# Optimization experiments

Hardware: AMD Instinct MI355X
Metric: run time of the kernel (lower is better)

Reference implementation:

```python
import jax, jax.numpy as jnp
import numpy as np

DIM = 2048
HEAD_DIM = 128
N_HEADS = 16
N_KV = 4
THETA = 10000.0
M = 2
B = 2
S = 2048


def _rope_table(seq_len, head_dim, theta):
    half = head_dim // 2
    inv_freq = 1.0 / (theta ** (jnp.arange(half, dtype=jnp.float32) * 2.0 / head_dim))
    ang = jnp.outer(jnp.arange(seq_len, dtype=jnp.float32), inv_freq)  # [S, half]
    cos, sin = jnp.cos(ang), jnp.sin(ang)
    # [S, half, 2, 2] rotation matrices: [[cos, -sin], [sin, cos]]
    return jnp.stack([jnp.stack([cos, -sin], axis=-1), jnp.stack([sin, cos], axis=-1)], axis=-2)


def setup_inputs() -> dict:
    key = jax.random.key(0)
    ks = jax.random.split(key, 6)
    std = DIM ** -0.5
    x = jax.random.normal(ks[0], (B, S, DIM), jnp.float32)
    Wq = jax.random.normal(ks[1], (M, DIM, N_HEADS * HEAD_DIM), jnp.float32) * std
    Wk = jax.random.normal(ks[2], (M, M, DIM, N_KV * HEAD_DIM), jnp.float32) * std
    Wv = jax.random.normal(ks[3], (M, M, DIM, N_KV * HEAD_DIM), jnp.float32) * std
    Wo = jax.random.normal(ks[4], (M, N_HEADS * HEAD_DIM, DIM), jnp.float32) * std
    modality_ids = jax.random.randint(ks[5], (B, S), 0, M, dtype=jnp.int32)
    freq_cis = _rope_table(S, HEAD_DIM, THETA)
    return {"x": x, "freq_cis": freq_cis, "Wq": Wq, "Wk": Wk, "Wv": Wv, "Wo": Wo,
            "modality_ids": modality_ids}


def _select_by_modality(all_proj, mid):
    # all_proj: [B, S, M, E]; mid: [B, S] int -> [B, S, E]
    Bb, Ss, Mm, E = all_proj.shape
    idx = jnp.broadcast_to(mid[:, :, None, None].astype(jnp.int32), (Bb, Ss, 1, E))
    return jnp.take_along_axis(all_proj, idx, axis=2)[:, :, 0]


def reference(x, freq_cis, Wq, Wk, Wv, Wo, modality_ids):
    Bb, Ss, D = x.shape
    mid = modality_ids

    # Per-modality Q projection, then per-token selection (gather/scatter in torch).
    q_all = jnp.einsum('bsd,mde->bsme', x, Wq)  # [B,S,M,H*hd]
    xq = _select_by_modality(q_all, mid)

    # In the original, xk[src token] accumulates wk[src_to_tgt](x) over ALL tgt,
    # which by linearity equals x @ sum_tgt(Wk[src, tgt]).
    Wk_sum = Wk.sum(axis=1)  # [M, D, Kh*hd]
    Wv_sum = Wv.sum(axis=1)
    k_all = jnp.einsum('bsd,mde->bsme', x, Wk_sum)
    v_all = jnp.einsum('bsd,mde->bsme', x, Wv_sum)
    xk = _select_by_modality(k_all, mid)
    xv = _select_by_modality(v_all, mid)

    xq = xq.reshape(Bb, Ss, N_HEADS, HEAD_DIM)
    xk = xk.reshape(Bb, Ss, N_KV, HEAD_DIM)
    xv = xv.reshape(Bb, Ss, N_KV, HEAD_DIM)

    # RoPE (positions = arange since tok_idx is None)
    F = freq_cis[:Ss]  # [S, hd/2, 2, 2]

    def rope(t):
        th = t.reshape(t.shape[0], t.shape[1], t.shape[2], HEAD_DIM // 2, 2)
        return jnp.einsum('bshdp,sdpq->bshdq', th, F).reshape(t.shape)

    xq = rope(xq)
    xk = rope(xk)

    # GQA repeat (interleaved, matching expand+reshape)
    rep = N_HEADS // N_KV
    xk = jnp.repeat(xk, rep, axis=2)
    xv = jnp.repeat(xv, rep, axis=2)

    q = xq.transpose(0, 2, 1, 3)  # [B,H,S,hd]
    k = xk.transpose(0, 2, 1, 3)
    v = xv.transpose(0, 2, 1, 3)

    scale = 1.0 / jnp.sqrt(jnp.asarray(HEAD_DIM, dtype=q.dtype))
    scores = jnp.einsum('bhqd,bhkd->bhqk', q, k) * scale
    attn = jax.nn.softmax(scores, axis=-1)
    out = jnp.einsum('bhqk,bhkd->bqhd', attn, v).reshape(Bb, Ss, N_HEADS * HEAD_DIM)

    # Per-modality output projection + selection
    o_all = jnp.einsum('bse,med->bsmd', out, Wo)  # [B,S,M,D]
    final = _select_by_modality(o_all, mid)
    return final
```

## Files before the change

### kernel.cpp

```cpp
#include <hip/hip_runtime.h>
#include <hip/hip_bf16.h>
#include <stdint.h>

typedef unsigned short u16;
typedef __attribute__((ext_vector_type(8))) __bf16 bf16x8;
typedef __attribute__((ext_vector_type(4))) float f32x4;
typedef __attribute__((ext_vector_type(8))) u16 us8;

#define QSCALE 0.08838834764831843f

__device__ __forceinline__ u16 f2bf(float f) {
  unsigned u = __float_as_uint(f);
  u += 0x7fffu + ((u >> 16) & 1u);
  return (u16)(u >> 16);
}
__device__ __forceinline__ float bf2f(u16 h) {
  return __uint_as_float(((unsigned)h) << 16);
}
__device__ __forceinline__ void gload16(const void* g, void* l) {
  __builtin_amdgcn_global_load_lds(
      (const __attribute__((address_space(1))) unsigned int*)g,
      (__attribute__((address_space(3))) unsigned int*)l, 16, 0, 0);
}

__global__ __launch_bounds__(256) void wprep(
    const float* __restrict__ Wq, const float* __restrict__ Wk,
    const float* __restrict__ Wv, const float* __restrict__ Wo,
    u16* __restrict__ WCT, u16* __restrict__ WOT) {
  const int sec = blockIdx.z;
  const float* s0;
  const float* s1 = nullptr;
  u16* dst;
  int N;
  switch (sec) {
    case 0: s0 = Wq;                 dst = WCT;               N = 2048; break;
    case 1: s0 = Wq + 2048*2048;     dst = WCT + 2048*2048;   N = 2048; break;
    case 2: s0 = Wk;                 s1 = Wk + 2048*512;      dst = WCT + 4096*2048; N = 512; break;
    case 3: s0 = Wk + 2*2048*512;    s1 = Wk + 3*2048*512;    dst = WCT + 4608*2048; N = 512; break;
    case 4: s0 = Wv;                 s1 = Wv + 2048*512;      dst = WCT + 5120*2048; N = 512; break;
    case 5: s0 = Wv + 2*2048*512;    s1 = Wv + 3*2048*512;    dst = WCT + 5632*2048; N = 512; break;
    case 6: s0 = Wo;                 dst = WOT;               N = 2048; break;
    default: s0 = Wo + 2048*2048;    dst = WOT + 2048*2048;   N = 2048; break;
  }
  const int n0 = blockIdx.x * 32;
  if (n0 >= N) return;
  const int k0 = blockIdx.y * 32;
  __shared__ float tile[32][33];
  const int tx = threadIdx.x & 31, ty = threadIdx.x >> 5;
#pragma unroll
  for (int i = 0; i < 4; ++i) {
    int k = k0 + ty + 8 * i;
    float v = s0[(size_t)k * N + n0 + tx];
    if (s1) v += s1[(size_t)k * N + n0 + tx];
    tile[ty + 8 * i][tx] = v;
  }
  __syncthreads();
#pragma unroll
  for (int i = 0; i < 4; ++i) {
    int n = n0 + ty + 8 * i;
    dst[(size_t)n * 2048 + k0 + tx] = f2bf(tile[tx][ty + 8 * i]);
  }
}

__global__ __launch_bounds__(256) void xcast(const float* __restrict__ x,
                                             u16* __restrict__ Xbf) {
  size_t base = ((size_t)blockIdx.x * 256 + threadIdx.x) * 8;
  float4 a = *(const float4*)&x[base];
  float4 c = *(const float4*)&x[base + 4];
  us8 o;
  o[0] = f2bf(a.x); o[1] = f2bf(a.y); o[2] = f2bf(a.z); o[3] = f2bf(a.w);
  o[4] = f2bf(c.x); o[5] = f2bf(c.y); o[6] = f2bf(c.z); o[7] = f2bf(c.w);
  *(us8*)&Xbf[base] = o;
}

__global__ __launch_bounds__(256) void gemm_bt(
    const u16* __restrict__ A, const u16* __restrict__ B, u16* __restrict__ C,
    int Mdim, int Ndim, int Kdim) {
  __shared__ u16 As[128 * 32];
  __shared__ u16 Bs[128 * 32];
  const int nbx = gridDim.x;
  const int nwg = nbx * gridDim.y;
  int bid = blockIdx.y * nbx + blockIdx.x;
  const int q = nwg >> 3;
  int swz = (bid & 7) * q + (bid >> 3);
  const int bx = swz % nbx, by = swz / nbx;
  const int row0 = by * 128, col0 = bx * 128;
  const int tid = threadIdx.x, wid = tid >> 6, lane = tid & 63;
  const int lr = lane & 15, lg = lane >> 4;
  const int wr = wid >> 1, wc = wid & 1;
  const u16* Abase = A + (size_t)row0 * Kdim;
  const u16* Bbase = B + (size_t)col0 * Kdim;

  f32x4 acc[4][4];
#pragma unroll
  for (int m = 0; m < 4; ++m)
#pragma unroll
    for (int n = 0; n < 4; ++n)
#pragma unroll
      for (int r = 0; r < 4; ++r) acc[m][n][r] = 0.f;

  for (int k0 = 0; k0 < Kdim; k0 += 32) {
#pragma unroll
    for (int j = 0; j < 2; ++j) {
      int c = j * 256 + wid * 64 + lane;
      int r = c >> 2, g = c & 3;
      gload16(Abase + (size_t)r * Kdim + k0 + g * 8, &As[(j * 256 + wid * 64) * 8]);
      gload16(Bbase + (size_t)r * Kdim + k0 + g * 8, &Bs[(j * 256 + wid * 64) * 8]);
    }
    __syncthreads();
    bf16x8 af[4], bfr[4];
#pragma unroll
    for (int m = 0; m < 4; ++m)
      af[m] = *(const bf16x8*)&As[(64 * wr + 16 * m + lr) * 32 + 8 * lg];
#pragma unroll
    for (int n = 0; n < 4; ++n)
      bfr[n] = *(const bf16x8*)&Bs[(64 * wc + 16 * n + lr) * 32 + 8 * lg];
#pragma unroll
    for (int m = 0; m < 4; ++m)
#pragma unroll
      for (int n = 0; n < 4; ++n)
        acc[m][n] = __builtin_amdgcn_mfma_f32_16x16x32_bf16(af[m], bfr[n], acc[m][n], 0, 0, 0);
    __syncthreads();
  }
#pragma unroll
  for (int m = 0; m < 4; ++m)
#pragma unroll
    for (int n = 0; n < 4; ++n)
#pragma unroll
      for (int r = 0; r < 4; ++r) {
        int grow = row0 + 64 * wr + 16 * m + 4 * lg + r;
        int gcol = col0 + 64 * wc + 16 * n + lr;
        C[(size_t)grow * Ndim + gcol] = f2bf(acc[m][n][r]);
      }
}

__global__ __launch_bounds__(256) void gemm_out(
    const u16* __restrict__ A, const u16* __restrict__ B,
    const int* __restrict__ mid, float* __restrict__ out) {
  __shared__ u16 As[128 * 32];
  __shared__ u16 Bs[128 * 32];
  const int nbx = gridDim.x;
  const int nwg = nbx * gridDim.y;
  int bid = blockIdx.y * nbx + blockIdx.x;
  const int q = nwg >> 3;
  int swz = (bid & 7) * q + (bid >> 3);
  const int bx = swz % nbx, by = swz / nbx;
  const int row0 = by * 128, col0 = bx * 128;
  const int tid = threadIdx.x, wid = tid >> 6, lane = tid & 63;
  const int lr = lane & 15, lg = lane >> 4;
  const int wr = wid >> 1, wc = wid & 1;
  const u16* Abase = A + (size_t)row0 * 2048;
  const u16* Bbase = B + (size_t)col0 * 2048;

  f32x4 acc[4][4];
#pragma unroll
  for (int m = 0; m < 4; ++m)
#pragma unroll
    for (int n = 0; n < 4; ++n)
#pragma unroll
      for (int r = 0; r < 4; ++r) acc[m][n][r] = 0.f;

  for (int k0 = 0; k0 < 2048; k0 += 32) {
#pragma unroll
    for (int j = 0; j < 2; ++j) {
      int c = j * 256 + wid * 64 + lane;
      int r = c >> 2, g = c & 3;
      gload16(Abase + (size_t)r * 2048 + k0 + g * 8, &As[(j * 256 + wid * 64) * 8]);
      gload16(Bbase + (size_t)r * 2048 + k0 + g * 8, &Bs[(j * 256 + wid * 64) * 8]);
    }
    __syncthreads();
    bf16x8 af[4], bfr[4];
#pragma unroll
    for (int m = 0; m < 4; ++m)
      af[m] = *(const bf16x8*)&As[(64 * wr + 16 * m + lr) * 32 + 8 * lg];
#pragma unroll
    for (int n = 0; n < 4; ++n)
      bfr[n] = *(const bf16x8*)&Bs[(64 * wc + 16 * n + lr) * 32 + 8 * lg];
#pragma unroll
    for (int m = 0; m < 4; ++m)
#pragma unroll
      for (int n = 0; n < 4; ++n)
        acc[m][n] = __builtin_amdgcn_mfma_f32_16x16x32_bf16(af[m], bfr[n], acc[m][n], 0, 0, 0);
    __syncthreads();
  }
#pragma unroll
  for (int m = 0; m < 4; ++m)
#pragma unroll
    for (int n = 0; n < 4; ++n)
#pragma unroll
      for (int r = 0; r < 4; ++r) {
        int grow = row0 + 64 * wr + 16 * m + 4 * lg + r;
        int gcol = col0 + 64 * wc + 16 * n + lr;
        int mod = gcol >> 11;
        if (mid[grow] == mod)
          out[(size_t)grow * 2048 + (gcol & 2047)] = acc[m][n][r];
      }
}

__global__ __launch_bounds__(256) void rope_select(
    const u16* __restrict__ QKV, const int* __restrict__ mid,
    const float* __restrict__ fc, u16* __restrict__ Qr, u16* __restrict__ Kr) {
  const int t = blockIdx.x;
  const int b = t >> 11, s = t & 2047;
  const int m = mid[t];
  __shared__ float Fs[256];
  Fs[threadIdx.x] = fc[(size_t)s * 256 + threadIdx.x];
  __syncthreads();
  const int tid = threadIdx.x;
  {
    int p0 = tid * 4;
    int h = p0 >> 6, ph0 = p0 & 63;
    const u16* src = QKV + (size_t)t * 6144 + m * 2048 + h * 128 + 2 * ph0;
    us8 v = *(const us8*)src;
    us8 o;
#pragma unroll
    for (int j = 0; j < 4; ++j) {
      float x0 = bf2f(v[2 * j]), x1 = bf2f(v[2 * j + 1]);
      const float* F = &Fs[(ph0 + j) * 4];
      o[2 * j]     = f2bf((x0 * F[0] + x1 * F[2]) * QSCALE);
      o[2 * j + 1] = f2bf((x0 * F[1] + x1 * F[3]) * QSCALE);
    }
    *(us8*)(Qr + (((size_t)(b * 16 + h) * 2048) + s) * 128 + 2 * ph0) = o;
  }
  if (tid < 64) {
    int p0 = tid * 4;
    int kh = p0 >> 6, ph0 = p0 & 63;
    const u16* src = QKV + (size_t)t * 6144 + 4096 + m * 512 + kh * 128 + 2 * ph0;
    us8 v = *(const us8*)src;
    us8 o;
#pragma unroll
    for (int j = 0; j < 4; ++j) {
      float x0 = bf2f(v[2 * j]), x1 = bf2f(v[2 * j + 1]);
      const float* F = &Fs[(ph0 + j) * 4];
      o[2 * j]     = f2bf(x0 * F[0] + x1 * F[2]);
      o[2 * j + 1] = f2bf(x0 * F[1] + x1 * F[3]);
    }
    *(us8*)(Kr + (((size_t)(b * 4 + kh) * 2048) + s) * 128 + 2 * ph0) = o;
  }
}

__global__ __launch_bounds__(256) void vtrans(
    const u16* __restrict__ QKV, const int* __restrict__ mid, u16* __restrict__ Vt) {
  __shared__ u16 tilebuf[32][34];
  const int s0 = blockIdx.x * 32, d0 = blockIdx.y * 32, b = blockIdx.z;
  const int tx = threadIdx.x & 31, ty = threadIdx.x >> 5;
#pragma unroll
  for (int i = 0; i < 4; ++i) {
    int s = s0 + ty + 8 * i;
    int t = b * 2048 + s;
    int m = mid[t];
    tilebuf[ty + 8 * i][tx] = QKV[(size_t)t * 6144 + 5120 + m * 512 + d0 + tx];
  }
  __syncthreads();
#pragma unroll
  for (int i = 0; i < 4; ++i) {
    int d = d0 + ty + 8 * i;
    Vt[(((size_t)(b * 4 + (d >> 7)) * 128) + (d & 127)) * 2048 + s0 + tx] =
        tilebuf[tx][ty + 8 * i];
  }
}

__global__ __launch_bounds__(256) void attn(
    const u16* __restrict__ Qr, const u16* __restrict__ Kr,
    const u16* __restrict__ Vt, u16* __restrict__ AO) {
  __shared__ u16 Ks[64 * 128];
  __shared__ u16 Vs[128 * 64];
  __shared__ u16 Ps[4][16 * 64];
  const int qb = blockIdx.x, h = blockIdx.y, b = blockIdx.z;
  const int kvh = h >> 2;
  const int tid = threadIdx.x, wid = tid >> 6, lane = tid & 63;
  const int lr = lane & 15, lg = lane >> 4;
  const u16* qp = Qr + (((size_t)(b * 16 + h) * 2048) + qb * 64 + 16 * wid) * 128;
  const u16* kp = Kr + ((size_t)(b * 4 + kvh) * 2048) * 128;
  const u16* vp = Vt + ((size_t)(b * 4 + kvh) * 128) * 2048;

  bf16x8 qf[4];
#pragma unroll
  for (int t4 = 0; t4 < 4; ++t4)
    qf[t4] = *(const bf16x8*)(qp + (size_t)lr * 128 + 32 * t4 + 8 * lg);

  f32x4 o[8];
#pragma unroll
  for (int i = 0; i < 8; ++i)
#pragma unroll
    for (int r = 0; r < 4; ++r) o[i][r] = 0.f;
  float mrow[4] = {-1e30f, -1e30f, -1e30f, -1e30f};
  float lrow[4] = {0.f, 0.f, 0.f, 0.f};

  for (int kb = 0; kb < 2048; kb += 64) {
#pragma unroll
    for (int j = 0; j < 4; ++j) {
      int c = j * 256 + wid * 64 + lane;
      int rk = c >> 4, gk = (c & 15) ^ (rk & 7);
      gload16(kp + (size_t)(kb + rk) * 128 + gk * 8, &Ks[(j * 256 + wid * 64) * 8]);
      int rv = c >> 3, gv = (c & 7) ^ (rv & 7);
      gload16(vp + (size_t)rv * 2048 + kb + gv * 8, &Vs[(j * 256 + wid * 64) * 8]);
    }
    __syncthreads();

    f32x4 s[4];
#pragma unroll
    for (int nf = 0; nf < 4; ++nf)
#pragma unroll
      for (int r = 0; r < 4; ++r) s[nf][r] = 0.f;
#pragma unroll
    for (int nf = 0; nf < 4; ++nf) {
      int R = 16 * nf + lr;
#pragma unroll
      for (int t4 = 0; t4 < 4; ++t4) {
        bf16x8 kf = *(const bf16x8*)&Ks[R * 128 + (((4 * t4 + lg) ^ (R & 7)) * 8)];
        s[nf] = __builtin_amdgcn_mfma_f32_16x16x32_bf16(qf[t4], kf, s[nf], 0, 0, 0);
      }
    }
    float sc[4];
#pragma unroll
    for (int r = 0; r < 4; ++r) {
      float mx = fmaxf(fmaxf(s[0][r], s[1][r]), fmaxf(s[2][r], s[3][r]));
      mx = fmaxf(mx, __shfl_xor(mx, 1));
      mx = fmaxf(mx, __shfl_xor(mx, 2));
      mx = fmaxf(mx, __shfl_xor(mx, 4));
      mx = fmaxf(mx, __shfl_xor(mx, 8));
      float mn = fmaxf(mrow[r], mx);
      sc[r] = __expf(mrow[r] - mn);
      float ps = 0.f;
#pragma unroll
      for (int nf = 0; nf < 4; ++nf) {
        float e = __expf(s[nf][r] - mn);
        s[nf][r] = e;
        ps += e;
      }
      ps += __shfl_xor(ps, 1);
      ps += __shfl_xor(ps, 2);
      ps += __shfl_xor(ps, 4);
      ps += __shfl_xor(ps, 8);
      lrow[r] = lrow[r] * sc[r] + ps;
      mrow[r] = mn;
    }
#pragma unroll
    for (int i = 0; i < 8; ++i)
#pragma unroll
      for (int r = 0; r < 4; ++r) o[i][r] *= sc[r];
    u16* pw = Ps[wid];
#pragma unroll
    for (int nf = 0; nf < 4; ++nf) {
      int cg = 2 * nf + (lr >> 3), ci = lr & 7;
#pragma unroll
      for (int r = 0; r < 4; ++r) {
        int prow = 4 * lg + r;
        pw[prow * 64 + ((cg ^ (prow & 7)) * 8) + ci] = f2bf(s[nf][r]);
      }
    }
#pragma unroll
    for (int ks = 0; ks < 2; ++ks) {
      bf16x8 pa = *(const bf16x8*)&pw[lr * 64 + (((4 * ks + lg) ^ (lr & 7)) * 8)];
#pragma unroll
      for (int n2 = 0; n2 < 8; ++n2) {
        int R2 = 16 * n2 + lr;
        bf16x8 vf = *(const bf16x8*)&Vs[R2 * 64 + (((4 * ks + lg) ^ (R2 & 7)) * 8)];
        o[n2] = __builtin_amdgcn_mfma_f32_16x16x32_bf16(pa, vf, o[n2], 0, 0, 0);
      }
    }
    __syncthreads();
  }
#pragma unroll
  for (int n2 = 0; n2 < 8; ++n2)
#pragma unroll
    for (int r = 0; r < 4; ++r) {
      int qrow = qb * 64 + 16 * wid + 4 * lg + r;
      AO[((size_t)(b * 2048) + qrow) * 2048 + h * 128 + 16 * n2 + lr] =
          f2bf(o[n2][r] / lrow[r]);
    }
}

extern "C" void kernel_launch(void* const* d_in, const int* in_sizes, int n_in,
                              void* d_out, int out_size, void* d_ws, size_t ws_size,
                              hipStream_t stream) {
  const float* x  = (const float*)d_in[0];
  const float* fc = (const float*)d_in[1];
  const float* Wq = (const float*)d_in[2];
  const float* Wk = (const float*)d_in[3];
  const float* Wv = (const float*)d_in[4];
  const float* Wo = (const float*)d_in[5];
  const int* mid  = (const int*)d_in[6];
  float* out = (float*)d_out;
  char* ws = (char*)d_ws;

  u16* XBF = (u16*)(ws);
  u16* WCT = (u16*)(ws + 16777216);
  u16* WOT = (u16*)(ws + 41943040);
  u16* QKV = (u16*)(ws + 58720256);
  u16* QR  = (u16*)(ws + 109051904);
  u16* KR  = (u16*)(ws + 125829120);
  u16* VT  = (u16*)(ws + 130023424);
  u16* AO  = (u16*)(ws + 134217728);
  if (ws_size < 150994944) return;

  wprep<<<dim3(64, 64, 8), dim3(256), 0, stream>>>(Wq, Wk, Wv, Wo, WCT, WOT);
  xcast<<<dim3(4096), dim3(256), 0, stream>>>(x, XBF);
  gemm_bt<<<dim3(48, 32), dim3(256), 0, stream>>>(XBF, WCT, QKV, 4096, 6144, 2048);
  rope_select<<<dim3(4096), dim3(256), 0, stream>>>(QKV, mid, fc, QR, KR);
  vtrans<<<dim3(64, 16, 2), dim3(256), 0, stream>>>(QKV, mid, VT);
  attn<<<dim3(32, 16, 2), dim3(256), 0, stream>>>(QR, KR, VT, AO);
  gemm_out<<<dim3(32, 32), dim3(256), 0, stream>>>(AO, WOT, mid, out);
}
```

Measured before the change: 613.3 us.

## Restructure attention with 32x32 MFMA, double-buffered KV, and register-resident P

Rewrites the attention kernel so each 512-thread block handles 256 queries (32 per wave), using 32x32x16 MFMAs with S computed transposed. P is kept in registers and exchanged via a lane-32 shuffle instead of going through LDS. K/V tiles are double-buffered so the next tile's loads overlap compute, and the running-max rescale is skipped when the new max stays within a threshold. Output is staged through LDS for coalesced stores. The cost is higher register and LDS pressure, and fewer blocks in the grid.

```diff
diff --git a/kernel.cpp b/kernel.cpp
--- a/kernel.cpp
+++ b/kernel.cpp
@@ -5,7 +5,9 @@
 typedef unsigned short u16;
 typedef __attribute__((ext_vector_type(8))) __bf16 bf16x8;
 typedef __attribute__((ext_vector_type(4))) float f32x4;
+typedef __attribute__((ext_vector_type(16))) float f32x16;
 typedef __attribute__((ext_vector_type(8))) u16 us8;
+typedef __attribute__((ext_vector_type(4))) unsigned u32x4;
 
 #define QSCALE 0.08838834764831843f
 
@@ -21,6 +23,9 @@
   __builtin_amdgcn_global_load_lds(
       (const __attribute__((address_space(1))) unsigned int*)g,
       (__attribute__((address_space(3))) unsigned int*)l, 16, 0, 0);
+}
+__device__ __forceinline__ unsigned sx32(unsigned v) {
+  return (unsigned)__shfl_xor((int)v, 32, 64);
 }
 
 __global__ __launch_bounds__(256) void wprep(
@@ -260,116 +265,149 @@
   }
 }
 
-__global__ __launch_bounds__(256) void attn(
+__global__ __launch_bounds__(512, 2) void attn(
     const u16* __restrict__ Qr, const u16* __restrict__ Kr,
     const u16* __restrict__ Vt, u16* __restrict__ AO) {
-  __shared__ u16 Ks[64 * 128];
-  __shared__ u16 Vs[128 * 64];
-  __shared__ u16 Ps[4][16 * 64];
-  const int qb = blockIdx.x, h = blockIdx.y, b = blockIdx.z;
-  const int kvh = h >> 2;
-  const int tid = threadIdx.x, wid = tid >> 6, lane = tid & 63;
-  const int lr = lane & 15, lg = lane >> 4;
-  const u16* qp = Qr + (((size_t)(b * 16 + h) * 2048) + qb * 64 + 16 * wid) * 128;
+  __shared__ u16 smem[34816];
+  u16* Kbuf[2] = { smem,          smem + 16384 };
+  u16* Vbuf[2] = { smem +  8192,  smem + 24576 };
+  Kbuf[0] = smem;          Vbuf[0] = smem + 8192;
+  Kbuf[1] = smem + 16384;  Vbuf[1] = smem + 24576;
+
+  const int qt = blockIdx.x, hd = blockIdx.y, b = blockIdx.z;
+  const int kvh = hd >> 2;
+  const int tid = threadIdx.x, wid = tid >> 6;
+  const int l31 = tid & 31, h = (tid >> 5) & 1;
+  const bool hi = h != 0;
+
+  const u16* qp = Qr + (((size_t)(b * 16 + hd) * 2048) + qt * 256 + wid * 32 + l31) * 128;
   const u16* kp = Kr + ((size_t)(b * 4 + kvh) * 2048) * 128;
   const u16* vp = Vt + ((size_t)(b * 4 + kvh) * 128) * 2048;
 
-  bf16x8 qf[4];
-#pragma unroll
-  for (int t4 = 0; t4 < 4; ++t4)
-    qf[t4] = *(const bf16x8*)(qp + (size_t)lr * 128 + 32 * t4 + 8 * lg);
-
-  f32x4 o[8];
-#pragma unroll
-  for (int i = 0; i < 8; ++i)
-#pragma unroll
-    for (int r = 0; r < 4; ++r) o[i][r] = 0.f;
-  float mrow[4] = {-1e30f, -1e30f, -1e30f, -1e30f};
-  float lrow[4] = {0.f, 0.f, 0.f, 0.f};
-
+  bf16x8 qf[8];
+#pragma unroll
+  for (int ds = 0; ds < 8; ++ds)
+    qf[ds] = *(const bf16x8*)(qp + 16 * ds + 8 * h);
+
+  f32x16 oacc[4];
+#pragma unroll
+  for (int dt = 0; dt < 4; ++dt)
+#pragma unroll
+    for (int r = 0; r < 16; ++r) oacc[dt][r] = 0.f;
+  float mrun = -1e30f, lrun = 0.f;
+
+#define STAGE_KV(KB, DK, DV)                                                   \
+  {                                                                            \
+    _Pragma("unroll") for (int j = 0; j < 2; ++j) {                            \
+      int c = j * 512 + tid;                                                   \
+      int rk = c >> 4, gk = (c & 15) ^ (rk & 7);                               \
+      gload16(kp + (size_t)((KB) + rk) * 128 + gk * 8,                         \
+              (DK) + (j * 512 + wid * 64) * 8);                                \
+      int rv = c >> 3, gv = (c & 7) ^ (rv & 7);                                \
+      gload16(vp + (size_t)rv * 2048 + (KB) + gv * 8,                          \
+              (DV) + (j * 512 + wid * 64) * 8);                                \
+    }                                                                          \
+  }
+
+  STAGE_KV(0, Kbuf[0], Vbuf[0]);
+  __syncthreads();
+
+  int cur = 0;
   for (int kb = 0; kb < 2048; kb += 64) {
-#pragma unroll
-    for (int j = 0; j < 4; ++j) {
-      int c = j * 256 + wid * 64 + lane;
-      int rk = c >> 4, gk = (c & 15) ^ (rk & 7);
-      gload16(kp + (size_t)(kb + rk) * 128 + gk * 8, &Ks[(j * 256 + wid * 64) * 8]);
-      int rv = c >> 3, gv = (c & 7) ^ (rv & 7);
-      gload16(vp + (size_t)rv * 2048 + kb + gv * 8, &Vs[(j * 256 + wid * 64) * 8]);
+    const u16* Kb = Kbuf[cur];
+    const u16* Vb = Vbuf[cur];
+    if (kb + 64 < 2048) STAGE_KV(kb + 64, Kbuf[cur ^ 1], Vbuf[cur ^ 1]);
+
+    f32x16 s0, s1;
+#pragma unroll
+    for (int r = 0; r < 16; ++r) { s0[r] = 0.f; s1[r] = 0.f; }
+    const int key0 = l31, key1 = 32 + l31;
+#pragma unroll
+    for (int ds = 0; ds < 8; ++ds) {
+      bf16x8 kf0 = *(const bf16x8*)&Kb[key0 * 128 + (((2 * ds + h) ^ (key0 & 7)) * 8)];
+      s0 = __builtin_amdgcn_mfma_f32_32x32x16_bf16(kf0, qf[ds], s0, 0, 0, 0);
+      bf16x8 kf1 = *(const bf16x8*)&Kb[key1 * 128 + (((2 * ds + h) ^ (key1 & 7)) * 8)];
+      s1 = __builtin_amdgcn_mfma_f32_32x32x16_bf16(kf1, qf[ds], s1, 0, 0, 0);
+    }
+
+    float pm = -1e30f;
+#pragma unroll
+    for (int r = 0; r < 16; ++r) pm = fmaxf(pm, fmaxf(s0[r], s1[r]));
+    pm = fmaxf(pm, __shfl_xor(pm, 32, 64));
+    if (!__all(pm <= mrun + 8.f)) {
+      float mn = fmaxf(mrun, pm);
+      float sc = __expf(mrun - mn);
+      mrun = mn;
+      lrun *= sc;
+#pragma unroll
+      for (int dt = 0; dt < 4; ++dt)
+#pragma unroll
+        for (int r = 0; r < 16; ++r) oacc[dt][r] *= sc;
+    }
+    float ls = 0.f;
+#pragma unroll
+    for (int r = 0; r < 16; ++r) { s0[r] = __expf(s0[r] - mrun); ls += s0[r]; }
+#pragma unroll
+    for (int r = 0; r < 16; ++r) { s1[r] = __expf(s1[r] - mrun); ls += s1[r]; }
+    ls += __shfl_xor(ls, 32, 64);
+    lrun += ls;
+
+    unsigned c[16];
+#pragma unroll
+    for (int j = 0; j < 8; ++j) {
+      asm("v_cvt_pk_bf16_f32 %0, %1, %2" : "=v"(c[j]) : "v"(s0[2 * j]), "v"(s0[2 * j + 1]));
+      asm("v_cvt_pk_bf16_f32 %0, %1, %2" : "=v"(c[8 + j]) : "v"(s1[2 * j]), "v"(s1[2 * j + 1]));
+    }
+
+#pragma unroll
+    for (int st = 0; st < 4; ++st) {
+      unsigned w0 = sx32(c[4 * st + 0]);
+      unsigned w1 = sx32(c[4 * st + 1]);
+      unsigned w2 = sx32(c[4 * st + 2]);
+      unsigned w3 = sx32(c[4 * st + 3]);
+      u32x4 pw;
+      pw.x = hi ? w2 : c[4 * st + 0];
+      pw.y = hi ? w3 : c[4 * st + 1];
+      pw.z = hi ? c[4 * st + 2] : w0;
+      pw.w = hi ? c[4 * st + 3] : w1;
+      union { u32x4 u; bf16x8 bf; } pc;
+      pc.u = pw;
+#pragma unroll
+      for (int dt = 0; dt < 4; ++dt) {
+        int d = 32 * dt + l31;
+        bf16x8 vf = *(const bf16x8*)&Vb[d * 64 + (((2 * st + h) ^ (d & 7)) * 8)];
+        oacc[dt] = __builtin_amdgcn_mfma_f32_32x32x16_bf16(vf, pc.bf, oacc[dt], 0, 0, 0);
+      }
     }
     __syncthreads();
-
-    f32x4 s[4];
-#pragma unroll
-    for (int nf = 0; nf < 4; ++nf)
-#pragma unroll
-      for (int r = 0; r < 4; ++r) s[nf][r] = 0.f;
-#pragma unroll
-    for (int nf = 0; nf < 4; ++nf) {
-      int R = 16 * nf + lr;
-#pragma unroll
-      for (int t4 = 0; t4 < 4; ++t4) {
-        bf16x8 kf = *(const bf16x8*)&Ks[R * 128 + (((4 * t4 + lg) ^ (R & 7)) * 8)];
-        s[nf] = __builtin_amdgcn_mfma_f32_16x16x32_bf16(qf[t4], kf, s[nf], 0, 0, 0);
-      }
-    }
-    float sc[4];
-#pragma unroll
-    for (int r = 0; r < 4; ++r) {
-      float mx = fmaxf(fmaxf(s[0][r], s[1][r]), fmaxf(s[2][r], s[3][r]));
-      mx = fmaxf(mx, __shfl_xor(mx, 1));
-      mx = fmaxf(mx, __shfl_xor(mx, 2));
-      mx = fmaxf(mx, __shfl_xor(mx, 4));
-      mx = fmaxf(mx, __shfl_xor(mx, 8));
-      float mn = fmaxf(mrow[r], mx);
-      sc[r] = __expf(mrow[r] - mn);
-      float ps = 0.f;
-#pragma unroll
-      for (int nf = 0; nf < 4; ++nf) {
-        float e = __expf(s[nf][r] - mn);
-        s[nf][r] = e;
-        ps += e;
-      }
-      ps += __shfl_xor(ps, 1);
-      ps += __shfl_xor(ps, 2);
-      ps += __shfl_xor(ps, 4);
-      ps += __shfl_xor(ps, 8);
-      lrow[r] = lrow[r] * sc[r] + ps;
-      mrow[r] = mn;
-    }
-#pragma unroll
-    for (int i = 0; i < 8; ++i)
-#pragma unroll
-      for (int r = 0; r < 4; ++r) o[i][r] *= sc[r];
-    u16* pw = Ps[wid];
-#pragma unroll
-    for (int nf = 0; nf < 4; ++nf) {
-      int cg = 2 * nf + (lr >> 3), ci = lr & 7;
-#pragma unroll
-      for (int r = 0; r < 4; ++r) {
-        int prow = 4 * lg + r;
-        pw[prow * 64 + ((cg ^ (prow & 7)) * 8) + ci] = f2bf(s[nf][r]);
-      }
-    }
-#pragma unroll
-    for (int ks = 0; ks < 2; ++ks) {
-      bf16x8 pa = *(const bf16x8*)&pw[lr * 64 + (((4 * ks + lg) ^ (lr & 7)) * 8)];
-#pragma unroll
-      for (int n2 = 0; n2 < 8; ++n2) {
-        int R2 = 16 * n2 + lr;
-        bf16x8 vf = *(const bf16x8*)&Vs[R2 * 64 + (((4 * ks + lg) ^ (R2 & 7)) * 8)];
-        o[n2] = __builtin_amdgcn_mfma_f32_16x16x32_bf16(pa, vf, o[n2], 0, 0, 0);
-      }
-    }
-    __syncthreads();
-  }
-#pragma unroll
-  for (int n2 = 0; n2 < 8; ++n2)
-#pragma unroll
-    for (int r = 0; r < 4; ++r) {
-      int qrow = qb * 64 + 16 * wid + 4 * lg + r;
-      AO[((size_t)(b * 2048) + qrow) * 2048 + h * 128 + 16 * n2 + lr] =
-          f2bf(o[n2][r] / lrow[r]);
-    }
+    cur ^= 1;
+  }
+
+  u16* Os = smem;
+  const float inv = 1.0f / lrun;
+  const int q = wid * 32 + l31;
+#pragma unroll
+  for (int dt = 0; dt < 4; ++dt)
+#pragma unroll
+    for (int a = 0; a < 4; ++a) {
+      int d = 32 * dt + 8 * a + 4 * h;
+      ushort4 w;
+      w.x = f2bf(oacc[dt][4 * a + 0] * inv);
+      w.y = f2bf(oacc[dt][4 * a + 1] * inv);
+      w.z = f2bf(oacc[dt][4 * a + 2] * inv);
+      w.w = f2bf(oacc[dt][4 * a + 3] * inv);
+      *(ushort4*)&Os[q * 136 + d] = w;
+    }
+  __syncthreads();
+  const size_t orow = (size_t)b * 2048 + qt * 256;
+#pragma unroll
+  for (int rep = 0; rep < 8; ++rep) {
+    int idx = rep * 512 + tid;
+    int qq = idx >> 4, g = idx & 15;
+    us8 v = *(const us8*)&Os[qq * 136 + g * 8];
+    *(us8*)&AO[(orow + qq) * 2048 + hd * 128 + g * 8] = v;
+  }
+#undef STAGE_KV
 }
 
 extern "C" void kernel_launch(void* const* d_in, const int* in_sizes, int n_in,
@@ -400,6 +438,6 @@
   gemm_bt<<<dim3(48, 32), dim3(256), 0, stream>>>(XBF, WCT, QKV, 4096, 6144, 2048);
   rope_select<<<dim3(4096), dim3(256), 0, stream>>>(QKV, mid, fc, QR, KR);
   vtrans<<<dim3(64, 16, 2), dim3(256), 0, stream>>>(QKV, mid, VT);
-  attn<<<dim3(32, 16, 2), dim3(256), 0, stream>>>(QR, KR, VT, AO);
+  attn<<<dim3(8, 16, 2), dim3(512), 0, stream>>>(QR, KR, VT, AO);
   gemm_out<<<dim3(32, 32), dim3(256), 0, stream>>>(AO, WOT, mid, out);
 }
```

After: 540.0 us. 1.14x faster.
